# Optimization experiments

Measured on AMD Instinct MI355X. Metric: run time of the kernel, lower is better.

The kernel has to match this reference:

```python
import jax, jax.numpy as jnp
import numpy as np


def _conv(x, w, b=None, stride=1, pad=0):
    # x: [N,C,H,W], w: [O,I,kh,kw]
    out = jax.lax.conv_general_dilated(
        x, w, (stride, stride), [(pad, pad), (pad, pad)],
        dimension_numbers=('NCHW', 'OIHW', 'NCHW'))
    return out if b is None else out + b[None, :, None, None]


def _cond_net(x, cw1, cb1, cw2, cb2, cw3, cb3):
    # ZeroPad2d(1) + conv(pad=0) == conv(pad=1)
    h = jax.nn.relu(_conv(x, cw1, cb1, stride=2, pad=1))
    h = jax.nn.relu(_conv(h, cw2, cb2, stride=2, pad=1))
    h = jax.nn.relu(_conv(h, cw3, cb3, stride=2, pad=1))
    return h.mean(axis=(2, 3))  # [B, 32]


def _hda(x, dyn_w, ow, share_w, share_b):
    # per-sample dynamic conv: weight[b] = dyn_w * ow[b]
    B = x.shape[0]
    w = dyn_w[None] * ow.reshape(B, *dyn_w.shape)  # [B,32,64,3,3]
    out1 = jax.vmap(lambda xb, wb: _conv(xb[None], wb, pad=1)[0])(x, w)
    out2 = _conv(x, share_w, share_b, pad=1)
    return jnp.concatenate([out1, out2], axis=1)  # [B,64,H,W]


def setup_inputs() -> dict:
    key = jax.random.key(0)
    ks = jax.random.split(key, 20)
    s = 0.05
    inp = {
        'x': jax.random.normal(ks[0], (8, 64, 256, 256), jnp.float32),
        'out_weight1': jax.random.normal(ks[1], (256, 64, 3, 3), jnp.float32),
        'out_weight2': jax.random.normal(ks[2], (256, 64, 3, 3), jnp.float32),
        # Condition_tp params
        'cw1': jax.random.normal(ks[3], (32, 64, 7, 7), jnp.float32) * s,
        'cb1': jnp.zeros((32,), jnp.float32),
        'cw2': jax.random.normal(ks[4], (32, 32, 3, 3), jnp.float32) * s,
        'cb2': jnp.zeros((32,), jnp.float32),
        'cw3': jax.random.normal(ks[5], (32, 32, 3, 3), jnp.float32) * s,
        'cb3': jnp.zeros((32,), jnp.float32),
        # FiLM linears (cond_nf=32 -> base_nf=64)
        'scale_w': jax.random.normal(ks[6], (64, 32), jnp.float32) * s,
        'scale_b': jnp.zeros((64,), jnp.float32),
        'shift_w': jax.random.normal(ks[7], (64, 32), jnp.float32) * s,
        'shift_b': jnp.zeros((64,), jnp.float32),
        # HDA_conv 1
        'dyn1_w': jax.random.normal(ks[8], (32, 64, 3, 3), jnp.float32) * s,
        'share1_w': jax.random.normal(ks[9], (32, 64, 3, 3), jnp.float32) * s,
        'share1_b': jnp.zeros((32,), jnp.float32),
        # HDA_conv 2
        'dyn2_w': jax.random.normal(ks[10], (32, 64, 3, 3), jnp.float32) * s,
        'share2_w': jax.random.normal(ks[11], (32, 64, 3, 3), jnp.float32) * s,
        'share2_b': jnp.zeros((32,), jnp.float32),
    }
    return inp


def reference(x, out_weight1, out_weight2, cw1, cb1, cw2, cb2, cw3, cb3,
              scale_w, scale_b, shift_w, shift_b,
              dyn1_w, share1_w, share1_b, dyn2_w, share2_w, share2_b):
    res_scale = 1.0
    cond = _cond_net(x, cw1, cb1, cw2, cb2, cw3, cb3)       # [B,32]
    scale = cond @ scale_w.T + scale_b                      # [B,64]
    shift = cond @ shift_w.T + shift_b                      # [B,64]
    out = _hda(x, dyn1_w, out_weight1, share1_w, share1_b)  # [B,64,H,W]
    # out*scale + shift + out  ==  out*(scale+1) + shift
    out = out * (scale[:, :, None, None] + 1.0) + shift[:, :, None, None]
    out = jax.nn.relu(out)
    out = _hda(out, dyn2_w, out_weight2, share2_w, share2_b)
    return x + out * res_scale
```

## Files before the change

### kernel.cpp

```cpp
#include <hip/hip_runtime.h>

typedef unsigned short u16;
typedef unsigned int u32;
typedef __attribute__((ext_vector_type(8))) __bf16 bf16x8;
typedef __attribute__((ext_vector_type(8))) u16 u16x8;
typedef __attribute__((ext_vector_type(4))) float f32x4;
typedef __attribute__((ext_vector_type(2))) u32 u32x2;

static constexpr size_t PSP = (size_t)8 * 258 * 258 * 16;

#define GPTR(p) ((const __attribute__((address_space(1))) void*)(p))
#define LPTR(p) ((__attribute__((address_space(3))) void*)(p))

__device__ __forceinline__ u16 f2bf(float f) {
  u32 u = __builtin_bit_cast(u32, f);
  u = (u + 0x7FFFu + ((u >> 16) & 1u)) >> 16;
  return (u16)u;
}

__device__ __forceinline__ f32x4 mfma16(bf16x8 a, bf16x8 b, f32x4 c) {
  return __builtin_amdgcn_mfma_f32_16x16x32_bf16(a, b, c, 0, 0, 0);
}

__global__ void k_zero_border(u16* __restrict__ base) {
  int idx = blockIdx.x * 256 + threadIdx.x;
  if (idx >= 4 * 8 * 1028) return;
  int p = idx / (8 * 1028), r = idx - p * (8 * 1028);
  int b = r / 1028, e = r - b * 1028;
  int y, x;
  if (e < 258) { y = 0; x = e; }
  else if (e < 516) { y = 257; x = e - 258; }
  else { int e2 = e - 516; y = 1 + (e2 >> 1); x = (e2 & 1) * 257; }
  u16* d = base + (size_t)p * PSP + (((size_t)b * 258 + y) * 258 + x) * 16;
  u16x8 z = (u16x8)0;
  *(u16x8*)d = z;
  *(u16x8*)(d + 8) = z;
}

__global__ __launch_bounds__(256) void k_tr(const float* __restrict__ x,
                                            u16* __restrict__ xh) {
  __shared__ float t[64][33];
  const int b = blockIdx.z, y = blockIdx.y, x0 = blockIdx.x * 32;
  const int tid = threadIdx.x;
  {
    int ic = tid >> 2, xo = (tid & 3) * 8;
    const float* s = x + (((size_t)b * 64 + ic) * 256 + y) * 256 + x0 + xo;
    f32x4 v0 = *(const f32x4*)s;
    f32x4 v1 = *(const f32x4*)(s + 4);
#pragma unroll
    for (int j = 0; j < 4; ++j) { t[ic][xo + j] = v0[j]; t[ic][xo + 4 + j] = v1[j]; }
  }
  __syncthreads();
  {
    int xc = tid & 31, slot = tid >> 5;
    int ic0 = slot * 8;
    u16x8 v;
#pragma unroll
    for (int j = 0; j < 8; ++j) v[j] = f2bf(t[ic0 + j][xc]);
    *(u16x8*)(xh + (size_t)(slot >> 1) * PSP +
              (((size_t)b * 258 + y + 1) * 258 + x0 + xc + 1) * 16 + (slot & 1) * 8) = v;
  }
}

__global__ void k_prep_cw(const float* __restrict__ src, u16* __restrict__ dst,
                          int IC, int KK2, int n, int perm) {
  int d = blockIdx.x * 256 + threadIdx.x;
  if (d >= n) return;
  int per = KK2 * IC;
  int oc = d / per, r = d - oc * per;
  int tap = r / IC, icp = r - tap * IC;
  int ic = perm ? ((icp >> 1) + (icp & 1) * 16) : icp;
  dst[d] = f2bf(src[(oc * IC + ic) * KK2 + tap]);
}

__global__ void k_prep_cw1(const float* __restrict__ src, u16* __restrict__ dst) {
  int d = blockIdx.x * 256 + threadIdx.x;
  if (d >= 106496) return;
  int h = d / 13312, r = d - h * 13312;
  int oc = r / 416, r2 = r - oc * 416;
  int tap = r2 >> 3, i = r2 & 7;
  float v = (tap < 49) ? src[(oc * 64 + h * 8 + i) * 49 + tap] : 0.f;
  dst[d] = f2bf(v);
}

__global__ void k_prep_hda(const float* __restrict__ dyn, const float* __restrict__ ow,
                           const float* __restrict__ share, const float* __restrict__ a_,
                           u16* __restrict__ dst, int use_a, int perm) {
  int d = blockIdx.x * 256 + threadIdx.x;
  if (d >= 327680) return;
  int b = d / 40960, r = d - b * 40960;
  int cc = r / 10240, r2 = r - cc * 10240;
  int oc = r2 / 160, r3 = r2 - oc * 160;
  int s = r3 >> 5, r4 = r3 & 31;
  int kq = r4 >> 3, j = r4 & 7;
  int tap = 2 * s + (kq >> 1);
  float v = 0.f;
  if (tap < 9) {
    int icp = cc * 16 + (kq & 1) * 8 + j;
    int ic = perm ? ((icp & 3) * 16 + (icp >> 2)) : icp;
    v = (oc < 32) ? dyn[(oc * 64 + ic) * 9 + tap] * ow[((b * 32 + oc) * 64 + ic) * 9 + tap]
                  : share[((oc - 32) * 64 + ic) * 9 + tap];
    if (use_a) v *= a_[b * 64 + oc];
  }
  dst[d] = f2bf(v);
}

__global__ __launch_bounds__(256, 3) void k_cond1_mfma(const u16* __restrict__ xh,
    const u16* __restrict__ wp , const float* __restrict__ cb,
    u16* __restrict__ dst) {
  __shared__ char lds[49664];
  const int wg0 = blockIdx.x;
  const int wg = ((wg0 & 7) << 6) | (wg0 >> 3);
  const int b = wg >> 6, rr = wg & 63;
  const int oh0 = (rr >> 3) << 4, ow0 = (rr & 7) << 4;
  const int tid = threadIdx.x, lane = tid & 63, wid = tid >> 6;
  const int col = lane & 15, kq = lane >> 4;
  const int ihs = 2 * oh0 - 1, iws = 2 * ow0 - 1;
  const u16x8 Z = (u16x8)0;
  f32x4 acc[4][2];
#pragma unroll
  for (int i = 0; i < 4; ++i)
#pragma unroll
    for (int j = 0; j < 2; ++j) acc[i][j] = 0.f;
  int pb[4];
#pragma unroll
  for (int mf = 0; mf < 4; ++mf) pb[mf] = (2 * (wid * 4 + mf)) * 37 + 2 * col;
  const int wl = 22528 + col * 848 + kq * 16;
#pragma unroll 1
  for (int h = 0; h < 8; ++h) {
    __syncthreads();
    for (int i = tid; i < 1406; i += 256) {
      int r = i / 37, cc = i - r * 37;
      int gy = ihs + r, gx = iws + cc;
      u16x8 v = Z;
      if ((unsigned)gy < 256u && (unsigned)gx < 256u)
        v = *(const u16x8*)(xh + (size_t)(h >> 1) * PSP +
                            (((size_t)b * 258 + gy + 1) * 258 + gx + 1) * 16 + (h & 1) * 8);
      *(u16x8*)(lds + (i ^ ((i >> 3) & 7)) * 16) = v;
    }
    for (int i = tid; i < 1664; i += 256) {
      int oc = i / 52, t = i - oc * 52;
      u16x8 v = *(const u16x8*)(wp + h * 13312 + oc * 416 + t * 8);
      *(u16x8*)(lds + 22528 + oc * 848 + t * 16) = v;
    }
    __syncthreads();
#pragma unroll
    for (int s = 0; s < 13; ++s) {
      const int t0 = 4 * s;
      const int kh0 = t0 / 7, r7 = t0 % 7;
      int carry = (kq >= 7 - r7) ? 1 : 0;
      int kh = kh0 + carry;
      int kw = r7 + kq - carry * 7;
      int prow = kh * 37 + kw;
      bf16x8 a[4];
#pragma unroll
      for (int mf = 0; mf < 4; ++mf) {
        int pos = pb[mf] + prow;
        int g = pos ^ ((pos >> 3) & 7);
        a[mf] = __builtin_bit_cast(bf16x8, *(const u16x8*)(lds + g * 16));
      }
      bf16x8 w[2];
#pragma unroll
      for (int nf = 0; nf < 2; ++nf)
        w[nf] = __builtin_bit_cast(bf16x8, *(const u16x8*)(lds + wl + nf * 13568 + s * 64));
#pragma unroll
      for (int mf = 0; mf < 4; ++mf)
#pragma unroll
        for (int nf = 0; nf < 2; ++nf) acc[mf][nf] = mfma16(a[mf], w[nf], acc[mf][nf]);
    }
  }
  const float bv0 = cb[col], bv1 = cb[16 + col];
#pragma unroll
  for (int mf = 0; mf < 4; ++mf) {
    int oh = oh0 + wid * 4 + mf;
    if (oh >= 126) continue;
#pragma unroll
    for (int r = 0; r < 4; ++r) {
      int ow = ow0 + kq * 4 + r;
      if (ow >= 126) continue;
      u32 pack = (u32)f2bf(fmaxf(acc[mf][0][r] + bv0, 0.f)) |
                 ((u32)f2bf(fmaxf(acc[mf][1][r] + bv1, 0.f)) << 16);
      *(u32*)(dst + (((size_t)b * 126 + oh) * 126 + ow) * 32 + col * 2) = pack;
    }
  }
}

template <int HI, int HO, int IC, int KK, int OUTF32>
__global__ __launch_bounds__(256, 4) void k_conv_s2(const u16* __restrict__ src,
    const u16* __restrict__ wgt, const float* __restrict__ bias, void* __restrict__ dst) {
  const int b = blockIdx.z;
  const int by0 = blockIdx.y * 8, bx0 = blockIdx.x * 16;
  const int tid = threadIdx.x, lane = tid & 63, wid = tid >> 6;
  const int col = lane & 15, kq = lane >> 4;
  f32x4 acc[2][2];
#pragma unroll
  for (int i = 0; i < 2; ++i)
#pragma unroll
    for (int j = 0; j < 2; ++j) acc[i][j] = 0.f;
  const u16x8 Z = (u16x8)0;
#pragma unroll
  for (int kh = 0; kh < KK; ++kh) {
#pragma unroll
    for (int kw = 0; kw < KK; ++kw) {
#pragma unroll
      for (int h = 0; h < IC / 32; ++h) {
        bf16x8 a[2];
#pragma unroll
        for (int mf = 0; mf < 2; ++mf) {
          int oh = by0 + wid * 2 + mf;
          int ih = 2 * oh - 1 + kh;
          int ix = 2 * (bx0 + col) - 1 + kw;
          int ic = h * 32 + kq * 8;
          u16x8 raw = Z;
          if ((unsigned)ih < (unsigned)HI && (unsigned)ix < (unsigned)HI)
            raw = *(const u16x8*)(src + (((size_t)b * HI + ih) * HI + ix) * IC + ic);
          a[mf] = __builtin_bit_cast(bf16x8, raw);
        }
        int k0 = (kh * KK + kw) * IC + h * 32 + kq * 8;
        bf16x8 w[2];
#pragma unroll
        for (int nf = 0; nf < 2; ++nf)
          w[nf] = __builtin_bit_cast(bf16x8,
                    *(const u16x8*)(wgt + (size_t)(nf * 16 + col) * (KK * KK * IC) + k0));
#pragma unroll
        for (int mf = 0; mf < 2; ++mf)
#pragma unroll
          for (int nf = 0; nf < 2; ++nf) acc[mf][nf] = mfma16(a[mf], w[nf], acc[mf][nf]);
      }
    }
  }
#pragma unroll
  for (int mf = 0; mf < 2; ++mf) {
    int oh = by0 + wid * 2 + mf;
    if (oh >= HO) continue;
#pragma unroll
    for (int nf = 0; nf < 2; ++nf) {
      int oc = nf * 16 + col;
      float bv = bias[oc];
#pragma unroll
      for (int r = 0; r < 4; ++r) {
        int ow = bx0 + kq * 4 + r;
        if (ow >= HO) continue;
        float v = fmaxf(acc[mf][nf][r] + bv, 0.f);
        if (OUTF32)
          ((float*)dst)[(((size_t)b * 32 + oc) * HO + oh) * HO + ow] = v;
        else
          ((u16*)dst)[(((size_t)b * HO + oh) * HO + ow) * 32 + oc] = f2bf(v);
      }
    }
  }
}

__global__ void k_mean(const float* __restrict__ h3, float* __restrict__ cond) {
  int bo = blockIdx.x;
  int tid = threadIdx.x;
  float s = 0.f;
  for (int i = tid; i < 1024; i += 256) s += h3[bo * 1024 + i];
  __shared__ float red[256];
  red[tid] = s;
  __syncthreads();
  for (int o = 128; o > 0; o >>= 1) {
    if (tid < o) red[tid] += red[tid + o];
    __syncthreads();
  }
  if (tid == 0) cond[bo] = red[0] * (1.f / 1024.f);
}

__global__ void k_film(const float* __restrict__ cond,
                       const float* __restrict__ scale_w, const float* __restrict__ scale_b,
                       const float* __restrict__ shift_w, const float* __restrict__ shift_b,
                       const float* __restrict__ share1_b, const float* __restrict__ share2_b,
                       float* __restrict__ a_, float* __restrict__ bias1,
                       float* __restrict__ bias2) {
  int t = threadIdx.x;
  int b = t >> 6, j = t & 63;
  float s = scale_b[j], sh = shift_b[j];
  for (int k = 0; k < 32; ++k) {
    float c = cond[b * 32 + k];
    s = fmaf(c, scale_w[j * 32 + k], s);
    sh = fmaf(c, shift_w[j * 32 + k], sh);
  }
  float a = s + 1.f;
  float b0 = (j < 32) ? 0.f : share1_b[j - 32];
  a_[t] = a;
  bias1[t] = fmaf(a, b0, sh);
  bias2[t] = (j < 32) ? 0.f : share2_b[j - 32];
}

__device__ __forceinline__ void hda_stage(const u16* __restrict__ asrc,
                                          const u16* __restrict__ wall,
                                          char* lb, int b, int by0, int bx0,
                                          int cc, int tid, int wid, int lane) {
  const u16* ap = asrc + (size_t)cc * PSP;
  const u16* wp = wall + (size_t)b * 40960 + cc * 10240;
#pragma unroll
  for (int it = 0; it < 3; ++it) {
    if (it < 2 || wid < 3) {
      int g = it * 256 + tid;
      int i = g ^ ((g >> 3) & 1);
      int pos = i >> 1, sl = i & 1;
      if (pos >= 342) { pos = 0; sl = 0; }
      int yy = pos / 18, xx = pos - yy * 18;
      const u16* src = ap + (((size_t)b * 258 + by0 + yy) * 258 + bx0 + xx) * 16 + sl * 8;
      __builtin_amdgcn_global_load_lds(GPTR(src), LPTR(lb + (it * 256 + wid * 64) * 16),
                                       16, 0, 0);
    }
  }
  for (int j = wid; j < 21; j += 4) {
    int gr = j * 64 + lane;
    int oc = gr / 21, t = gr - oc * 21;
    if (t > 19) t = 19;
    const u16* src = wp + oc * 160 + t * 8;
    __builtin_amdgcn_global_load_lds(GPTR(src), LPTR(lb + 11264 + j * 1024), 16, 0, 0);
  }
}

template <int STAGE>
__global__ __launch_bounds__(256, 2) void k_hda_mfma(const u16* __restrict__ asrc,
    const u16* __restrict__ wall, const float* __restrict__ bias,
    const float* __restrict__ resid, void* __restrict__ dst) {
  __shared__ char lds[65536];
  const int wg0 = blockIdx.x;
  const int wg = ((wg0 & 7) << 8) + (wg0 >> 3);
  const int b = wg >> 8;
  const int rr = wg & 255;
  const int by0 = (rr >> 4) << 4, bx0 = (rr & 15) << 4;
  const int tid = threadIdx.x, lane = tid & 63, wid = tid >> 6;
  const int col = lane & 15, kq = lane >> 4;
  const int hi = kq >> 1, sl2 = kq & 1;
  f32x4 acc[4][4];
#pragma unroll
  for (int i = 0; i < 4; ++i)
#pragma unroll
    for (int j = 0; j < 4; ++j) acc[i][j] = 0.f;
  hda_stage(asrc, wall, lds, b, by0, bx0, 0, tid, wid, lane);
#pragma unroll
  for (int cc = 0; cc < 4; ++cc) {
    __syncthreads();
    if (cc < 3)
      hda_stage(asrc, wall, lds + ((cc + 1) & 1) * 32768, b, by0, bx0, cc + 1,
                tid, wid, lane);
    char* lb = lds + (cc & 1) * 32768;
#pragma unroll
    for (int s = 0; s < 5; ++s) {
      const int t0 = 2 * s, t1 = 2 * s + 1;
      const int d0 = (t0 / 3) * 18 + (t0 % 3);
      const int d1 = (t1 / 3) * 18 + (t1 % 3);
      const int dd = hi ? d1 : d0;
      bf16x8 a[4];
#pragma unroll
      for (int mf = 0; mf < 4; ++mf) {
        int pos = (wid * 4 + mf) * 18 + col + dd;
        int g = (pos * 2 + sl2) ^ ((pos >> 2) & 1);
        a[mf] = __builtin_bit_cast(bf16x8, *(const u16x8*)(lb + g * 16));
      }
      bf16x8 w[4];
#pragma unroll
      for (int nf = 0; nf < 4; ++nf)
        w[nf] = __builtin_bit_cast(bf16x8,
            *(const u16x8*)(lb + 11264 + (nf * 16 + col) * 336 + (s * 4 + kq) * 16));
#pragma unroll
      for (int mf = 0; mf < 4; ++mf)
#pragma unroll
        for (int nf = 0; nf < 4; ++nf) acc[mf][nf] = mfma16(a[mf], w[nf], acc[mf][nf]);
    }
  }
  const float* bb = bias + b * 64;
#pragma unroll
  for (int mf = 0; mf < 4; ++mf) {
    int y = by0 + wid * 4 + mf;
    if (STAGE == 1) {
#pragma unroll
      for (int r = 0; r < 4; ++r) {
        int x = bx0 + kq * 4 + r;
        u32x2 pk;
        pk[0] = (u32)f2bf(fmaxf(acc[mf][0][r] + bb[col], 0.f)) |
                ((u32)f2bf(fmaxf(acc[mf][1][r] + bb[16 + col], 0.f)) << 16);
        pk[1] = (u32)f2bf(fmaxf(acc[mf][2][r] + bb[32 + col], 0.f)) |
                ((u32)f2bf(fmaxf(acc[mf][3][r] + bb[48 + col], 0.f)) << 16);
        *(u32x2*)((u16*)dst + (size_t)(col >> 2) * PSP +
                  (((size_t)b * 258 + y + 1) * 258 + x + 1) * 16 + (col & 3) * 4) = pk;
      }
    } else {
#pragma unroll
      for (int nf = 0; nf < 4; ++nf) {
        int oc = nf * 16 + col;
        float bv = bb[oc];
        size_t o = (((size_t)b * 64 + oc) * 256 + y) * 256 + bx0 + kq * 4;
        f32x4 rx = *(const f32x4*)(resid + o);
        f32x4 vv;
#pragma unroll
        for (int r = 0; r < 4; ++r) vv[r] = rx[r] + acc[mf][nf][r] + bv;
        *(f32x4*)((float*)dst + o) = vv;
      }
    }
  }
}

extern "C" void kernel_launch(void* const* d_in, const int* in_sizes, int n_in,
                              void* d_out, int out_size, void* d_ws, size_t ws_size,
                              hipStream_t stream) {
  const float* x        = (const float*)d_in[0];
  const float* ow1      = (const float*)d_in[1];
  const float* ow2      = (const float*)d_in[2];
  const float* cw1      = (const float*)d_in[3];
  const float* cb1      = (const float*)d_in[4];
  const float* cw2      = (const float*)d_in[5];
  const float* cb2      = (const float*)d_in[6];
  const float* cw3      = (const float*)d_in[7];
  const float* cb3      = (const float*)d_in[8];
  const float* scale_w  = (const float*)d_in[9];
  const float* scale_b  = (const float*)d_in[10];
  const float* shift_w  = (const float*)d_in[11];
  const float* shift_b  = (const float*)d_in[12];
  const float* dyn1     = (const float*)d_in[13];
  const float* share1   = (const float*)d_in[14];
  const float* share1_b = (const float*)d_in[15];
  const float* dyn2     = (const float*)d_in[16];
  const float* share2   = (const float*)d_in[17];
  const float* share2_b = (const float*)d_in[18];
  float* out = (float*)d_out;

  char* p = (char*)d_ws;
  u16* xh   = (u16*)p;            p += PSP * 4 * 2;
  u16* midh = (u16*)p;            p += PSP * 4 * 2;
  u16* wbf1 = (u16*)p;            p += (size_t)327680 * 2;
  u16* wbf2 = (u16*)p;            p += (size_t)327680 * 2;
  u16* cwb1 = (u16*)p;            p += (size_t)106496 * 2;
  u16* cwb2 = (u16*)p;            p += (size_t)32 * 288 * 2;
  u16* cwb3 = (u16*)p;            p += (size_t)32 * 288 * 2;
  float* a_    = (float*)p;       p += 512 * 4;
  float* bias1 = (float*)p;       p += 512 * 4;
  float* bias2 = (float*)p;       p += 512 * 4;
  float* cond  = (float*)p;       p += 256 * 4;
  u16* h1h = midh;
  u16* h2h = h1h + (size_t)8 * 126 * 126 * 32;
  float* h3 = (float*)(h2h + (size_t)8 * 63 * 63 * 32);

  k_zero_border<<<129, 256, 0, stream>>>(xh);
  k_tr<<<dim3(8, 256, 8), 256, 0, stream>>>(x, xh);

  k_prep_cw1<<<(106496 + 255) / 256, 256, 0, stream>>>(cw1, cwb1);
  k_prep_cw<<<(32 * 288 + 255) / 256, 256, 0, stream>>>(cw2, cwb2, 32, 9, 32 * 288, 1);
  k_prep_cw<<<(32 * 288 + 255) / 256, 256, 0, stream>>>(cw3, cwb3, 32, 9, 32 * 288, 0);

  k_cond1_mfma<<<512, 256, 0, stream>>>(xh, cwb1, cb1, h1h);
  k_conv_s2<126, 63, 32, 3, 0><<<dim3(4, 8, 8), 256, 0, stream>>>(h1h, cwb2, cb2, h2h);
  k_conv_s2<63, 32, 32, 3, 1><<<dim3(2, 4, 8), 256, 0, stream>>>(h2h, cwb3, cb3, h3);

  k_mean<<<256, 256, 0, stream>>>(h3, cond);
  k_film<<<1, 512, 0, stream>>>(cond, scale_w, scale_b, shift_w, shift_b,
                                share1_b, share2_b, a_, bias1, bias2);

  k_zero_border<<<129, 256, 0, stream>>>(midh);

  k_prep_hda<<<(327680 + 255) / 256, 256, 0, stream>>>(dyn1, ow1, share1, a_, wbf1, 1, 0);
  k_prep_hda<<<(327680 + 255) / 256, 256, 0, stream>>>(dyn2, ow2, share2, a_, wbf2, 0, 1);

  k_hda_mfma<1><<<2048, 256, 0, stream>>>(xh, wbf1, bias1, nullptr, midh);
  k_hda_mfma<2><<<2048, 256, 0, stream>>>(midh, wbf2, bias2, x, out);
}
```

Before: 270.5 us.

## Stage cond1 conv tiles with direct global-to-LDS loads and raise MFMA wave priority

```diff
diff --git a/kernel.cpp b/kernel.cpp
--- a/kernel.cpp
+++ b/kernel.cpp
@@ -77,9 +77,9 @@
   int d = blockIdx.x * 256 + threadIdx.x;
   if (d >= 106496) return;
   int h = d / 13312, r = d - h * 13312;
-  int oc = r / 416, r2 = r - oc * 416;
-  int tap = r2 >> 3, i = r2 & 7;
-  float v = (tap < 49) ? src[(oc * 64 + h * 8 + i) * 49 + tap] : 0.f;
+  int t = r >> 8, r2 = r & 255;
+  int oc = r2 >> 3, i = r2 & 7;
+  float v = (t < 49) ? src[(oc * 64 + h * 8 + i) * 49 + t] : 0.f;
   dst[d] = f2bf(v);
 }
 
@@ -105,18 +105,16 @@
   dst[d] = f2bf(v);
 }
 
-__global__ __launch_bounds__(256, 3) void k_cond1_mfma(const u16* __restrict__ xh,
+__global__ __launch_bounds__(256, 2) void k_cond1_mfma(const u16* __restrict__ xh,
     const u16* __restrict__ wp , const float* __restrict__ cb,
     u16* __restrict__ dst) {
-  __shared__ char lds[49664];
+  __shared__ char lds[49152];
   const int wg0 = blockIdx.x;
   const int wg = ((wg0 & 7) << 6) | (wg0 >> 3);
   const int b = wg >> 6, rr = wg & 63;
   const int oh0 = (rr >> 3) << 4, ow0 = (rr & 7) << 4;
   const int tid = threadIdx.x, lane = tid & 63, wid = tid >> 6;
   const int col = lane & 15, kq = lane >> 4;
-  const int ihs = 2 * oh0 - 1, iws = 2 * ow0 - 1;
-  const u16x8 Z = (u16x8)0;
   f32x4 acc[4][2];
 #pragma unroll
   for (int i = 0; i < 4; ++i)
@@ -125,25 +123,34 @@
   int pb[4];
 #pragma unroll
   for (int mf = 0; mf < 4; ++mf) pb[mf] = (2 * (wid * 4 + mf)) * 37 + 2 * col;
-  const int wl = 22528 + col * 848 + kq * 16;
 #pragma unroll 1
   for (int h = 0; h < 8; ++h) {
     __syncthreads();
-    for (int i = tid; i < 1406; i += 256) {
-      int r = i / 37, cc = i - r * 37;
-      int gy = ihs + r, gx = iws + cc;
-      u16x8 v = Z;
-      if ((unsigned)gy < 256u && (unsigned)gx < 256u)
-        v = *(const u16x8*)(xh + (size_t)(h >> 1) * PSP +
-                            (((size_t)b * 258 + gy + 1) * 258 + gx + 1) * 16 + (h & 1) * 8);
-      *(u16x8*)(lds + (i ^ ((i >> 3) & 7)) * 16) = v;
-    }
-    for (int i = tid; i < 1664; i += 256) {
-      int oc = i / 52, t = i - oc * 52;
-      u16x8 v = *(const u16x8*)(wp + h * 13312 + oc * 416 + t * 8);
-      *(u16x8*)(lds + 22528 + oc * 848 + t * 16) = v;
+#pragma unroll
+    for (int it = 0; it < 6; ++it) {
+      if (it < 5 || wid < 2) {
+        int g = it * 256 + tid;
+        int i = g ^ ((g >> 3) & 7);
+        if (i >= 1406) i = 0;
+        int r = i / 37, cc2 = i - r * 37;
+        const u16* src = xh + (size_t)(h >> 1) * PSP +
+            (((size_t)b * 258 + 2 * oh0 + r) * 258 + 2 * ow0 + cc2) * 16 + (h & 1) * 8;
+        __builtin_amdgcn_global_load_lds(GPTR(src),
+            LPTR(lds + (it * 256 + wid * 64) * 16), 16, 0, 0);
+      }
+    }
+#pragma unroll
+    for (int it = 0; it < 7; ++it) {
+      if (it < 6 || wid < 2) {
+        int g = it * 256 + tid;
+        int t = g >> 5, oc = g & 31;
+        const u16* src = wp + h * 13312 + t * 256 + oc * 8;
+        __builtin_amdgcn_global_load_lds(GPTR(src),
+            LPTR(lds + 22528 + (it * 256 + wid * 64) * 16), 16, 0, 0);
+      }
     }
     __syncthreads();
+    __builtin_amdgcn_s_setprio(1);
 #pragma unroll
     for (int s = 0; s < 13; ++s) {
       const int t0 = 4 * s;
@@ -162,12 +169,14 @@
       bf16x8 w[2];
 #pragma unroll
       for (int nf = 0; nf < 2; ++nf)
-        w[nf] = __builtin_bit_cast(bf16x8, *(const u16x8*)(lds + wl + nf * 13568 + s * 64));
+        w[nf] = __builtin_bit_cast(bf16x8,
+            *(const u16x8*)(lds + 22528 + (((4 * s + kq) * 32) + nf * 16 + col) * 16));
 #pragma unroll
       for (int mf = 0; mf < 4; ++mf)
 #pragma unroll
         for (int nf = 0; nf < 2; ++nf) acc[mf][nf] = mfma16(a[mf], w[nf], acc[mf][nf]);
     }
+    __builtin_amdgcn_s_setprio(0);
   }
   const float bv0 = cb[col], bv1 = cb[16 + col];
 #pragma unroll
@@ -341,6 +350,7 @@
       hda_stage(asrc, wall, lds + ((cc + 1) & 1) * 32768, b, by0, bx0, cc + 1,
                 tid, wid, lane);
     char* lb = lds + (cc & 1) * 32768;
+    __builtin_amdgcn_s_setprio(1);
 #pragma unroll
     for (int s = 0; s < 5; ++s) {
       const int t0 = 2 * s, t1 = 2 * s + 1;
@@ -364,6 +374,7 @@
 #pragma unroll
         for (int nf = 0; nf < 4; ++nf) acc[mf][nf] = mfma16(a[mf], w[nf], acc[mf][nf]);
     }
+    __builtin_amdgcn_s_setprio(0);
   }
   const float* bb = bias + b * 64;
 #pragma unroll
```

Result: faster. 251.3 us (-7.1%).
